# Kernel tuning notes

Hardware: AMD Instinct MI355X
Metric: run time of the kernel (lower is better)

Reference implementation:

```python
import jax, jax.numpy as jnp
from jax import lax
import numpy as np

B, S, HID = 1, 1024, 4096
H, D = 64, 64  # num_heads, head_size (hidden = H*D)


def setup_inputs() -> dict:
    key = jax.random.key(0)
    ks = jax.random.split(key, 14)
    s = 0.02  # weight init scale
    return {
        "hidden": jax.random.normal(ks[0], (B, S, HID), jnp.float32),
        "w_key": jax.random.normal(ks[1], (HID, HID), jnp.float32) * s,
        "w_value": jax.random.normal(ks[2], (HID, HID), jnp.float32) * s,
        "w_receptance": jax.random.normal(ks[3], (HID, HID), jnp.float32) * s,
        "w_gate": jax.random.normal(ks[4], (HID, HID), jnp.float32) * s,
        "w_output": jax.random.normal(ks[5], (HID, HID), jnp.float32) * s,
        "time_mix_key": jax.random.uniform(ks[6], (HID,), jnp.float32),
        "time_mix_value": jax.random.uniform(ks[7], (HID,), jnp.float32),
        "time_mix_receptance": jax.random.uniform(ks[8], (HID,), jnp.float32),
        "time_mix_gate": jax.random.uniform(ks[9], (HID,), jnp.float32),
        "time_decay": jax.random.normal(ks[10], (H, D), jnp.float32) * 0.5,
        "time_faaaa": jax.random.normal(ks[11], (H, D), jnp.float32) * 0.5,
        "gn_weight": jnp.ones((HID,), jnp.float32),
        "gn_bias": jnp.zeros((HID,), jnp.float32),
    }


def reference(hidden, w_key, w_value, w_receptance, w_gate, w_output,
              time_mix_key, time_mix_value, time_mix_receptance, time_mix_gate,
              time_decay, time_faaaa, gn_weight, gn_bias):
    b, s, hid = hidden.shape
    h, d = time_decay.shape

    # time_shift: shifted[t] = hidden[t-1], shifted[0] = 0 (state is None)
    shifted = jnp.concatenate([jnp.zeros_like(hidden[:, :1]), hidden[:, :-1]], axis=1)

    def mix(m):
        return hidden * m + shifted * (1.0 - m)

    k = mix(time_mix_key) @ w_key.T            # (b, s, hid)
    v = mix(time_mix_value) @ w_value.T
    r = mix(time_mix_receptance) @ w_receptance.T
    g = jax.nn.silu(mix(time_mix_gate) @ w_gate.T)

    def heads(x):  # (b, s, hid) -> (s, b, h, d) for scan over time
        return x.reshape(b, s, h, d).transpose(1, 0, 2, 3)

    kh, vh, rh = heads(k), heads(v), heads(r)

    td = jnp.exp(-jnp.exp(time_decay))[None, :, :, None]  # (1, h, d, 1)
    tf = time_faaaa[None, :, :, None]                      # (1, h, d, 1)

    def step(state, rkv):
        r_t, k_t, v_t = rkv                                # each (b, h, d)
        a = k_t[..., :, None] * v_t[..., None, :]          # (b, h, d, d) outer product
        o = jnp.einsum('bhd,bhde->bhe', r_t, tf * a + state)
        return a + td * state, o

    state0 = jnp.zeros((b, h, d, d), jnp.float32)
    _, out = lax.scan(step, state0, (rh, kh, vh))          # out: (s, b, h, d)
    out = out.transpose(1, 0, 2, 3).reshape(b, s, hid)

    # GroupNorm(num_groups=h, channels=hid) over flattened tokens
    x = out.reshape(b * s, h, d)
    mu = x.mean(-1, keepdims=True)
    var = x.var(-1, keepdims=True)
    xn = (x - mu) * lax.rsqrt(var + 1e-5)
    xn = xn.reshape(b * s, hid) * gn_weight + gn_bias
    xn = xn.reshape(b, s, hid)

    return (g * xn) @ w_output.T
```

## Files before the change

### kernel.cpp

```cpp
#include <hip/hip_runtime.h>

#define S_LEN 1024
#define HIDN  4096
#define NH    64
#define HD    64
#define NCH   32
#define CLEN  32
#define NKT   64

typedef short bf16x8 __attribute__((ext_vector_type(8)));
typedef float f32x4  __attribute__((ext_vector_type(4)));

__device__ __forceinline__ unsigned short f2bf(float x){
  unsigned u = __float_as_uint(x);
  u += 0x7fffu + ((u >> 16) & 1u);
  return (unsigned short)(u >> 16);
}

__device__ __forceinline__ void gload_lds16(const void* g, void* l){
  __builtin_amdgcn_global_load_lds(
      (const __attribute__((address_space(1))) void*)g,
      (__attribute__((address_space(3))) void*)l, 16, 0, 0);
}

#define SBAR() do { __builtin_amdgcn_sched_barrier(0); \
                    __builtin_amdgcn_s_barrier();      \
                    __builtin_amdgcn_sched_barrier(0); } while(0)
#define WAIT_LGKM0() do { asm volatile("s_waitcnt lgkmcnt(0)" ::: "memory"); \
                          __builtin_amdgcn_sched_barrier(0); } while(0)
#define WAIT_VM4()  do { asm volatile("s_waitcnt vmcnt(4)" ::: "memory"); \
                         __builtin_amdgcn_sched_barrier(0); } while(0)
#define WAIT_VM0()  do { asm volatile("s_waitcnt vmcnt(0)" ::: "memory"); \
                         __builtin_amdgcn_sched_barrier(0); } while(0)

__global__ __launch_bounds__(256)
void wconv_kernel(const float* __restrict__ w0, const float* __restrict__ w1,
                  const float* __restrict__ w2, const float* __restrict__ w3,
                  const float* __restrict__ w4, unsigned short* __restrict__ out)
{
  const int z = blockIdx.y;
  const float* __restrict__ w = (z==0)?w0:(z==1)?w1:(z==2)?w2:(z==3)?w3:w4;
  const size_t idx = (size_t)blockIdx.x * 2048 + (size_t)threadIdx.x * 8;
  float4 a = *(const float4*)(w + idx);
  float4 b = *(const float4*)(w + idx + 4);
  ushort4 lo, hi;
  lo.x = f2bf(a.x); lo.y = f2bf(a.y); lo.z = f2bf(a.z); lo.w = f2bf(a.w);
  hi.x = f2bf(b.x); hi.y = f2bf(b.y); hi.z = f2bf(b.z); hi.w = f2bf(b.w);
  unsigned short* o = out + (size_t)z * HIDN * HIDN + idx;
  *(ushort4*)(o)     = lo;
  *(ushort4*)(o + 4) = hi;
}

__global__ __launch_bounds__(256)
void mix_kernel(const float* __restrict__ hidden,
                const float* __restrict__ tmk, const float* __restrict__ tmv,
                const float* __restrict__ tmr, const float* __restrict__ tmg,
                unsigned short* __restrict__ mixed)
{
  int idx = blockIdx.x * 256 + threadIdx.x;
  int i = idx & (HIDN - 1);
  float h  = hidden[idx];
  float sh = (idx >= HIDN) ? hidden[idx - HIDN] : 0.f;
  float mk = tmk[i], mv = tmv[i], mr = tmr[i], mg = tmg[i];
  mixed[idx + 0 * S_LEN * HIDN] = f2bf(h * mk + sh * (1.f - mk));
  mixed[idx + 1 * S_LEN * HIDN] = f2bf(h * mv + sh * (1.f - mv));
  mixed[idx + 2 * S_LEN * HIDN] = f2bf(h * mr + sh * (1.f - mr));
  mixed[idx + 3 * S_LEN * HIDN] = f2bf(h * mg + sh * (1.f - mg));
}

__global__ __launch_bounds__(512, 2)
void gemm256(const unsigned short* __restrict__ Aall,
             const unsigned short* __restrict__ Wall,
             float* __restrict__ Call, int silu_mask)
{
  const int bid  = blockIdx.x;
  const int xcd  = bid & 7;
  const int slot = bid >> 3;
  const int nz   = xcd * 8 + (slot >> 2);
  const int mt   = slot & 3;
  const int z    = nz >> 4;
  const int nt   = nz & 15;
  const int m0 = mt * 256, n0 = nt * 256;

  const unsigned short* __restrict__ A = Aall + (size_t)z * S_LEN * HIDN;
  const unsigned short* __restrict__ W = Wall + (size_t)z * HIDN * HIDN;
  float* __restrict__ C = Call + (size_t)z * S_LEN * HIDN;

  __shared__ __align__(16) unsigned short As[2][2][128 * 64];
  __shared__ __align__(16) unsigned short Bs[2][2][128 * 64];

  const int tid  = threadIdx.x;
  const int lane = tid & 63;
  const int wid  = tid >> 6;
  const int wr   = wid >> 2;
  const int wc   = wid & 3;
  const int fr   = lane & 15;
  const int fku  = lane >> 4;
  const int cxA  = fku * 16;

  const int ob0 = tid * 16, ob1 = (512 + tid) * 16;
  const int r0 = ob0 >> 7, r1 = ob1 >> 7;
  const int cb0 = (ob0 & 127) ^ ((r0 & 7) << 4);
  const int cb1 = (ob1 & 127) ^ ((r1 & 7) << 4);
  const unsigned short* A0 = A + (size_t)(m0 + r0) * HIDN + (cb0 >> 1);
  const unsigned short* A1 = A + (size_t)(m0 + r1) * HIDN + (cb1 >> 1);
  const unsigned short* W0 = W + (size_t)(n0 + r0) * HIDN + (cb0 >> 1);
  const unsigned short* W1 = W + (size_t)(n0 + r1) * HIDN + (cb1 >> 1);
  const int lo0 = ob0 >> 1, lo1 = ob1 >> 1;

  f32x4 acc[8][4];
#pragma unroll
  for (int mi = 0; mi < 8; ++mi)
#pragma unroll
    for (int ni = 0; ni < 4; ++ni) acc[mi][ni] = (f32x4){0.f, 0.f, 0.f, 0.f};

  auto stageA = [&](int t, int h, int db) {
    gload_lds16(A0 + (size_t)h * 128 * HIDN + t * 64, &As[db][h][lo0]);
    gload_lds16(A1 + (size_t)h * 128 * HIDN + t * 64, &As[db][h][lo1]);
  };
  auto stageB = [&](int t, int h, int db) {
    gload_lds16(W0 + (size_t)h * 128 * HIDN + t * 64, &Bs[db][h][lo0]);
    gload_lds16(W1 + (size_t)h * 128 * HIDN + t * 64, &Bs[db][h][lo1]);
  };
  auto readA = [&](bf16x8 (&a)[2][4], int db, int mh) {
#pragma unroll
    for (int kk = 0; kk < 2; ++kk)
#pragma unroll
      for (int mi = 0; mi < 4; ++mi) {
        int rr  = mh * 64 + mi * 16 + fr;
        int byo = rr * 128 + ((kk * 64 + cxA) ^ ((rr & 7) << 4));
        a[kk][mi] = *(const bf16x8*)((const char*)As[db][wr] + byo);
      }
  };
  auto readB = [&](bf16x8 (&b)[2][2], int db, int nh) {
#pragma unroll
    for (int kk = 0; kk < 2; ++kk)
#pragma unroll
      for (int ni = 0; ni < 2; ++ni) {
        int rr  = (wc & 1) * 64 + nh * 32 + ni * 16 + fr;
        int byo = rr * 128 + ((kk * 64 + cxA) ^ ((rr & 7) << 4));
        b[kk][ni] = *(const bf16x8*)((const char*)Bs[db][wc >> 1] + byo);
      }
  };
  auto quad = [&](bf16x8 (&a)[2][4], bf16x8 (&b)[2][2], int mh, int nh) {
#pragma unroll
    for (int kk = 0; kk < 2; ++kk)
#pragma unroll
      for (int mi = 0; mi < 4; ++mi)
#pragma unroll
        for (int ni = 0; ni < 2; ++ni)
          acc[mh * 4 + mi][nh * 2 + ni] = __builtin_amdgcn_mfma_f32_16x16x32_bf16(
              a[kk][mi], b[kk][ni], acc[mh * 4 + mi][nh * 2 + ni], 0, 0, 0);
  };

  stageB(0, 0, 0); stageB(0, 1, 0);
  stageA(0, 0, 0); stageA(0, 1, 0);
  stageB(1, 0, 1); stageB(1, 1, 1);
  WAIT_VM4();
  SBAR();

  bf16x8 a8[2][4], b0[2][2], b1[2][2];

  for (int T = 0; T < NKT; ++T) {
    const int db  = T & 1;
    const int dbA = (T + 1) & 1;
    const int tA  = (T + 1 < NKT) ? T + 1 : NKT - 1;
    const int tB  = (T + 2 < NKT) ? T + 2 : NKT - 1;
    readA(a8, db, 0);
    readB(b0, db, 0);
    stageA(tA, 0, dbA);
    SBAR();
    WAIT_LGKM0();
    __builtin_amdgcn_s_setprio(1);
    quad(a8, b0, 0, 0);
    __builtin_amdgcn_s_setprio(0);
    SBAR();
    readB(b1, db, 1);
    stageA(tA, 1, dbA);
    SBAR();
    WAIT_LGKM0();
    __builtin_amdgcn_s_setprio(1);
    quad(a8, b1, 0, 1);
    __builtin_amdgcn_s_setprio(0);
    SBAR();
    readA(a8, db, 1);
    stageB(tB, 0, db);
    SBAR();
    WAIT_LGKM0();
    __builtin_amdgcn_s_setprio(1);
    quad(a8, b1, 1, 1);
    __builtin_amdgcn_s_setprio(0);
    SBAR();
    stageB(tB, 1, db);
    WAIT_VM4();
    SBAR();
    __builtin_amdgcn_s_setprio(1);
    quad(a8, b0, 1, 0);
    __builtin_amdgcn_s_setprio(0);
    SBAR();
  }
  WAIT_VM0();

  const bool do_silu = (silu_mask >> z) & 1;
  const int orow = fku * 4;
#pragma unroll
  for (int mi = 0; mi < 8; ++mi)
#pragma unroll
    for (int ni = 0; ni < 4; ++ni)
#pragma unroll
      for (int r = 0; r < 4; ++r) {
        int row = m0 + wr * 128 + mi * 16 + orow + r;
        int col = n0 + wc * 64 + ni * 16 + fr;
        float v = acc[mi][ni][r];
        if (do_silu) v = v / (1.f + __expf(-v));
        C[(size_t)row * HIDN + col] = v;
      }
}

__global__ __launch_bounds__(256)
void gemm_splitk(const unsigned short* __restrict__ A,
                 const unsigned short* __restrict__ W,
                 float* __restrict__ C)
{
  const int bid  = blockIdx.x;
  const int xcd  = bid & 7;
  const int slot = bid >> 3;
  const int mt   = slot & 7;
  const int nl   = (slot >> 3) & 3;
  const int ks   = slot >> 5;
  const int nt   = xcd * 4 + nl;
  const int m0 = mt * 128, n0 = nt * 128;
  const int kb = ks * (HIDN / 2), ke = kb + (HIDN / 2);

  __shared__ unsigned short As[2][128 * 32];
  __shared__ unsigned short Bs[2][128 * 32];

  const int tid  = threadIdx.x;
  const int lane = tid & 63;
  const int wave = tid >> 6;
  const int wr = (wave >> 1) * 64;
  const int wc = (wave & 1) * 64;
  const int fr = lane & 15;
  const int fk = (lane >> 4) * 8;

  const int q0 = tid, q1 = 256 + tid;
  const int r0 = q0 >> 2, c0 = (q0 & 3) * 8;
  const int r1 = q1 >> 2, c1 = (q1 & 3) * 8;
  const unsigned short* A0 = A + (size_t)(m0 + r0) * HIDN + c0;
  const unsigned short* A1 = A + (size_t)(m0 + r1) * HIDN + c1;
  const unsigned short* W0 = W + (size_t)(n0 + r0) * HIDN + c0;
  const unsigned short* W1 = W + (size_t)(n0 + r1) * HIDN + c1;

  f32x4 acc[4][4];
#pragma unroll
  for (int mi = 0; mi < 4; ++mi)
#pragma unroll
    for (int ni = 0; ni < 4; ++ni) acc[mi][ni] = (f32x4){0.f, 0.f, 0.f, 0.f};

  for (int k0 = kb; k0 < ke; k0 += 64) {
    gload_lds16(A0 + k0,      &As[0][q0 * 8]);
    gload_lds16(A1 + k0,      &As[0][q1 * 8]);
    gload_lds16(A0 + k0 + 32, &As[1][q0 * 8]);
    gload_lds16(A1 + k0 + 32, &As[1][q1 * 8]);
    gload_lds16(W0 + k0,      &Bs[0][q0 * 8]);
    gload_lds16(W1 + k0,      &Bs[0][q1 * 8]);
    gload_lds16(W0 + k0 + 32, &Bs[1][q0 * 8]);
    gload_lds16(W1 + k0 + 32, &Bs[1][q1 * 8]);
    __syncthreads();

#pragma unroll
    for (int kk = 0; kk < 2; ++kk) {
      bf16x8 af[4], bq[4];
#pragma unroll
      for (int mi = 0; mi < 4; ++mi)
        af[mi] = *(const bf16x8*)(&As[kk][(wr + mi * 16 + fr) * 32 + fk]);
#pragma unroll
      for (int ni = 0; ni < 4; ++ni)
        bq[ni] = *(const bf16x8*)(&Bs[kk][(wc + ni * 16 + fr) * 32 + fk]);
#pragma unroll
      for (int mi = 0; mi < 4; ++mi)
#pragma unroll
        for (int ni = 0; ni < 4; ++ni)
          acc[mi][ni] = __builtin_amdgcn_mfma_f32_16x16x32_bf16(af[mi], bq[ni], acc[mi][ni], 0, 0, 0);
    }
    __syncthreads();
  }

  const int orow = (lane >> 4) * 4;
#pragma unroll
  for (int mi = 0; mi < 4; ++mi)
#pragma unroll
    for (int ni = 0; ni < 4; ++ni)
#pragma unroll
      for (int r = 0; r < 4; ++r) {
        int row = m0 + wr + mi * 16 + orow + r;
        int col = n0 + wc + ni * 16 + fr;
        atomicAdd(&C[(size_t)row * HIDN + col], acc[mi][ni][r]);
      }
}

__global__ __launch_bounds__(64)
void rec_pass1(const float* __restrict__ kb, const float* __restrict__ vb,
               const float* __restrict__ time_decay, float* __restrict__ X)
{
  const int c = blockIdx.x, h = blockIdx.y, e = threadIdx.x;
  const float tde = __expf(-__expf(time_decay[h * 64 + e]));
  float td[64];
#pragma unroll
  for (int d = 0; d < 64; ++d) td[d] = __shfl(tde, d, 64);
  float st[64];
#pragma unroll
  for (int d = 0; d < 64; ++d) st[d] = 0.f;

  for (int t = c * CLEN; t < c * CLEN + CLEN; ++t) {
    const size_t off = (size_t)t * HIDN + h * 64;
    const float vl = vb[off + e];
    const float* __restrict__ krow = kb + off;
#pragma unroll
    for (int d = 0; d < 64; ++d)
      st[d] = fmaf(td[d], st[d], krow[d] * vl);
  }
#pragma unroll
  for (int d = 0; d < 64; ++d)
    X[(((size_t)c * NH + h) * 64 + d) * 64 + e] = st[d];
}

__global__ __launch_bounds__(64)
void rec_pass2(const float* __restrict__ time_decay,
               const float* __restrict__ X, float* __restrict__ Y)
{
  const int h = blockIdx.x, dq = blockIdx.y, e = threadIdx.x;
  float tdc[16];
#pragma unroll
  for (int i = 0; i < 16; ++i)
    tdc[i] = __expf(-(float)CLEN * __expf(time_decay[h * 64 + dq * 16 + i]));
  float acc[16];
#pragma unroll
  for (int i = 0; i < 16; ++i) acc[i] = 0.f;
  for (int c = 0; c < NCH; ++c) {
#pragma unroll
    for (int i = 0; i < 16; ++i) {
      size_t idx = (((size_t)c * NH + h) * 64 + dq * 16 + i) * 64 + e;
      Y[idx] = acc[i];
      acc[i] = fmaf(tdc[i], acc[i], X[idx]);
    }
  }
}

__global__ __launch_bounds__(64)
void rec_pass3(const float* __restrict__ kb, const float* __restrict__ vb,
               const float* __restrict__ rb, const float* __restrict__ gb,
               const float* __restrict__ time_decay, const float* __restrict__ time_faaaa,
               const float* __restrict__ gnw, const float* __restrict__ gnb,
               const float* __restrict__ Y, unsigned short* __restrict__ A2)
{
  const int c = blockIdx.x, h = blockIdx.y, e = threadIdx.x;
  const float tde = __expf(-__expf(time_decay[h * 64 + e]));
  float td[64];
#pragma unroll
  for (int d = 0; d < 64; ++d) td[d] = __shfl(tde, d, 64);
  float st[64];
#pragma unroll
  for (int d = 0; d < 64; ++d)
    st[d] = Y[(((size_t)c * NH + h) * 64 + d) * 64 + e];

  const float tf_l  = time_faaaa[h * 64 + e];
  const float gnw_l = gnw[h * 64 + e];
  const float gnb_l = gnb[h * 64 + e];

  for (int t = c * CLEN; t < c * CLEN + CLEN; ++t) {
    const size_t off = (size_t)t * HIDN + h * 64;
    const float kl = kb[off + e], rl = rb[off + e];
    const float vl = vb[off + e], gl = gb[off + e];

    float Asum = rl * tf_l * kl;
#pragma unroll
    for (int i = 1; i < 64; i <<= 1) Asum += __shfl_xor(Asum, i, 64);

    const float* __restrict__ krow = kb + off;
    const float* __restrict__ rrow = rb + off;
    float dot = 0.f;
#pragma unroll
    for (int d = 0; d < 64; ++d) {
      dot   = fmaf(rrow[d], st[d], dot);
      st[d] = fmaf(td[d], st[d], krow[d] * vl);
    }
    float o = fmaf(Asum, vl, dot);

    float s1 = o, s2 = o * o;
#pragma unroll
    for (int i = 1; i < 64; i <<= 1) {
      s1 += __shfl_xor(s1, i, 64);
      s2 += __shfl_xor(s2, i, 64);
    }
    float mean = s1 * (1.f / 64.f);
    float var  = s2 * (1.f / 64.f) - mean * mean;
    float xn   = (o - mean) * rsqrtf(var + 1e-5f);
    float yv   = xn * gnw_l + gnb_l;
    A2[off + e] = f2bf(gl * yv);
  }
}

extern "C" void kernel_launch(void* const* d_in, const int* in_sizes, int n_in,
                              void* d_out, int out_size, void* d_ws, size_t ws_size,
                              hipStream_t stream)
{
  const float* hidden     = (const float*)d_in[0];
  const float* w_key      = (const float*)d_in[1];
  const float* w_value    = (const float*)d_in[2];
  const float* w_recep    = (const float*)d_in[3];
  const float* w_gate     = (const float*)d_in[4];
  const float* w_output   = (const float*)d_in[5];
  const float* tmk        = (const float*)d_in[6];
  const float* tmv        = (const float*)d_in[7];
  const float* tmr        = (const float*)d_in[8];
  const float* tmg        = (const float*)d_in[9];
  const float* time_decay = (const float*)d_in[10];
  const float* time_faaaa = (const float*)d_in[11];
  const float* gnw        = (const float*)d_in[12];
  const float* gnb        = (const float*)d_in[13];
  float* out = (float*)d_out;

  char* ws = (char*)d_ws;
  unsigned short* wbf   = (unsigned short*)(ws);
  float*          Y     = (float*)(ws);
  unsigned short* mixed = (unsigned short*)(ws + 167772160);
  float*          X     = (float*)(ws + 167772160);
  float*          kvrg  = (float*)(ws + 201326592);
  unsigned short* A2    = (unsigned short*)(ws + 268435456);

  const float* kb = kvrg + 0 * (size_t)S_LEN * HIDN;
  const float* vb = kvrg + 1 * (size_t)S_LEN * HIDN;
  const float* rb = kvrg + 2 * (size_t)S_LEN * HIDN;
  const float* gb = kvrg + 3 * (size_t)S_LEN * HIDN;

  wconv_kernel<<<dim3(HIDN * HIDN / 2048, 5), 256, 0, stream>>>(
      w_key, w_value, w_recep, w_gate, w_output, wbf);

  mix_kernel<<<dim3(S_LEN * HIDN / 256), 256, 0, stream>>>(hidden, tmk, tmv, tmr, tmg, mixed);

  gemm256<<<dim3(256), 512, 0, stream>>>(mixed, wbf, kvrg, 0x8);

  rec_pass1<<<dim3(NCH, NH), 64, 0, stream>>>(kb, vb, time_decay, X);
  rec_pass2<<<dim3(NH, 4), 64, 0, stream>>>(time_decay, X, Y);
  rec_pass3<<<dim3(NCH, NH), 64, 0, stream>>>(kb, vb, rb, gb, time_decay, time_faaaa,
                                              gnw, gnb, Y, A2);

  hipMemsetAsync(d_out, 0, (size_t)out_size * sizeof(float), stream);
  gemm_splitk<<<dim3(512), 256, 0, stream>>>(A2, wbf + 4 * (size_t)HIDN * HIDN, out);
}
```

Measured before the change: 675.9 us.

## Reuse pipelined 256x256 GEMM body for split-K output projection and relax waits

Factors the 256x256 MFMA GEMM into a templated body that takes a K-tile count and an atomic-accumulate flag. The output projection now runs through it with 4-way split-K (16 K-tiles per block, atomicAdd epilogue), replacing the simpler 128x128 split-K kernel that synchronised twice per K step. The per-quad LDS waits and extra barriers in the main loop are removed and the vmcnt wait moves to the end of each iteration, aiming for more overlap of MFMA with LDS reads. Dropping the lgkmcnt waits leaves it to the compiler to place waits for the LDS reads, and the extra split-K partitions add atomic traffic.

New measurement: 690.3 us. 2.1% more time.

```diff
diff --git a/kernel.cpp b/kernel.cpp
--- a/kernel.cpp
+++ b/kernel.cpp
@@ -6,7 +6,6 @@
 #define HD    64
 #define NCH   32
 #define CLEN  32
-#define NKT   64
 
 typedef short bf16x8 __attribute__((ext_vector_type(8)));
 typedef float f32x4  __attribute__((ext_vector_type(4)));
@@ -26,12 +25,8 @@
 #define SBAR() do { __builtin_amdgcn_sched_barrier(0); \
                     __builtin_amdgcn_s_barrier();      \
                     __builtin_amdgcn_sched_barrier(0); } while(0)
-#define WAIT_LGKM0() do { asm volatile("s_waitcnt lgkmcnt(0)" ::: "memory"); \
-                          __builtin_amdgcn_sched_barrier(0); } while(0)
-#define WAIT_VM4()  do { asm volatile("s_waitcnt vmcnt(4)" ::: "memory"); \
-                         __builtin_amdgcn_sched_barrier(0); } while(0)
-#define WAIT_VM0()  do { asm volatile("s_waitcnt vmcnt(0)" ::: "memory"); \
-                         __builtin_amdgcn_sched_barrier(0); } while(0)
+#define WAIT_VM4()  do { asm volatile("s_waitcnt vmcnt(4)" ::: "memory"); } while(0)
+#define WAIT_VM0()  do { asm volatile("s_waitcnt vmcnt(0)" ::: "memory"); } while(0)
 
 __global__ __launch_bounds__(256)
 void wconv_kernel(const float* __restrict__ w0, const float* __restrict__ w1,
@@ -68,24 +63,11 @@
   mixed[idx + 3 * S_LEN * HIDN] = f2bf(h * mg + sh * (1.f - mg));
 }
 
-__global__ __launch_bounds__(512, 2)
-void gemm256(const unsigned short* __restrict__ Aall,
-             const unsigned short* __restrict__ Wall,
-             float* __restrict__ Call, int silu_mask)
-{
-  const int bid  = blockIdx.x;
-  const int xcd  = bid & 7;
-  const int slot = bid >> 3;
-  const int nz   = xcd * 8 + (slot >> 2);
-  const int mt   = slot & 3;
-  const int z    = nz >> 4;
-  const int nt   = nz & 15;
-  const int m0 = mt * 256, n0 = nt * 256;
-
-  const unsigned short* __restrict__ A = Aall + (size_t)z * S_LEN * HIDN;
-  const unsigned short* __restrict__ W = Wall + (size_t)z * HIDN * HIDN;
-  float* __restrict__ C = Call + (size_t)z * S_LEN * HIDN;
-
+template<int KTILES, bool ATOMIC>
+__device__ __forceinline__ void gemm_body(
+    const unsigned short* __restrict__ A, const unsigned short* __restrict__ W,
+    float* __restrict__ C, int m0, int n0, int kbase, bool do_silu)
+{
   __shared__ __align__(16) unsigned short As[2][2][128 * 64];
   __shared__ __align__(16) unsigned short Bs[2][2][128 * 64];
 
@@ -102,10 +84,10 @@
   const int r0 = ob0 >> 7, r1 = ob1 >> 7;
   const int cb0 = (ob0 & 127) ^ ((r0 & 7) << 4);
   const int cb1 = (ob1 & 127) ^ ((r1 & 7) << 4);
-  const unsigned short* A0 = A + (size_t)(m0 + r0) * HIDN + (cb0 >> 1);
-  const unsigned short* A1 = A + (size_t)(m0 + r1) * HIDN + (cb1 >> 1);
-  const unsigned short* W0 = W + (size_t)(n0 + r0) * HIDN + (cb0 >> 1);
-  const unsigned short* W1 = W + (size_t)(n0 + r1) * HIDN + (cb1 >> 1);
+  const unsigned short* A0 = A + (size_t)(m0 + r0) * HIDN + kbase + (cb0 >> 1);
+  const unsigned short* A1 = A + (size_t)(m0 + r1) * HIDN + kbase + (cb1 >> 1);
+  const unsigned short* W0 = W + (size_t)(n0 + r0) * HIDN + kbase + (cb0 >> 1);
+  const unsigned short* W1 = W + (size_t)(n0 + r1) * HIDN + kbase + (cb1 >> 1);
   const int lo0 = ob0 >> 1, lo1 = ob1 >> 1;
 
   f32x4 acc[8][4];
@@ -161,47 +143,39 @@
 
   bf16x8 a8[2][4], b0[2][2], b1[2][2];
 
-  for (int T = 0; T < NKT; ++T) {
+  for (int T = 0; T < KTILES; ++T) {
     const int db  = T & 1;
-    const int dbA = (T + 1) & 1;
-    const int tA  = (T + 1 < NKT) ? T + 1 : NKT - 1;
-    const int tB  = (T + 2 < NKT) ? T + 2 : NKT - 1;
+    const int dbA = db ^ 1;
+    const int tA  = (T + 1 < KTILES) ? T + 1 : T;
+    const int tB  = (T + 2 < KTILES) ? T + 2 : T;
     readA(a8, db, 0);
     readB(b0, db, 0);
     stageA(tA, 0, dbA);
-    SBAR();
-    WAIT_LGKM0();
     __builtin_amdgcn_s_setprio(1);
     quad(a8, b0, 0, 0);
     __builtin_amdgcn_s_setprio(0);
     SBAR();
     readB(b1, db, 1);
     stageA(tA, 1, dbA);
-    SBAR();
-    WAIT_LGKM0();
     __builtin_amdgcn_s_setprio(1);
     quad(a8, b1, 0, 1);
     __builtin_amdgcn_s_setprio(0);
     SBAR();
     readA(a8, db, 1);
     stageB(tB, 0, db);
-    SBAR();
-    WAIT_LGKM0();
     __builtin_amdgcn_s_setprio(1);
     quad(a8, b1, 1, 1);
     __builtin_amdgcn_s_setprio(0);
     SBAR();
     stageB(tB, 1, db);
-    WAIT_VM4();
-    SBAR();
     __builtin_amdgcn_s_setprio(1);
     quad(a8, b0, 1, 0);
     __builtin_amdgcn_s_setprio(0);
+    WAIT_VM4();
     SBAR();
   }
   WAIT_VM0();
 
-  const bool do_silu = (silu_mask >> z) & 1;
   const int orow = fku * 4;
 #pragma unroll
   for (int mi = 0; mi < 8; ++mi)
@@ -212,91 +186,45 @@
         int row = m0 + wr * 128 + mi * 16 + orow + r;
         int col = n0 + wc * 64 + ni * 16 + fr;
         float v = acc[mi][ni][r];
-        if (do_silu) v = v / (1.f + __expf(-v));
-        C[(size_t)row * HIDN + col] = v;
+        if (ATOMIC) {
+          atomicAdd(&C[(size_t)row * HIDN + col], v);
+        } else {
+          if (do_silu) v = v / (1.f + __expf(-v));
+          C[(size_t)row * HIDN + col] = v;
+        }
       }
 }
 
-__global__ __launch_bounds__(256)
-void gemm_splitk(const unsigned short* __restrict__ A,
-                 const unsigned short* __restrict__ W,
-                 float* __restrict__ C)
+__global__ __launch_bounds__(512, 2)
+void gemm_main(const unsigned short* __restrict__ Aall,
+               const unsigned short* __restrict__ Wall,
+               float* __restrict__ Call, int silu_mask)
 {
   const int bid  = blockIdx.x;
   const int xcd  = bid & 7;
   const int slot = bid >> 3;
-  const int mt   = slot & 7;
-  const int nl   = (slot >> 3) & 3;
-  const int ks   = slot >> 5;
-  const int nt   = xcd * 4 + nl;
-  const int m0 = mt * 128, n0 = nt * 128;
-  const int kb = ks * (HIDN / 2), ke = kb + (HIDN / 2);
-
-  __shared__ unsigned short As[2][128 * 32];
-  __shared__ unsigned short Bs[2][128 * 32];
-
-  const int tid  = threadIdx.x;
-  const int lane = tid & 63;
-  const int wave = tid >> 6;
-  const int wr = (wave >> 1) * 64;
-  const int wc = (wave & 1) * 64;
-  const int fr = lane & 15;
-  const int fk = (lane >> 4) * 8;
-
-  const int q0 = tid, q1 = 256 + tid;
-  const int r0 = q0 >> 2, c0 = (q0 & 3) * 8;
-  const int r1 = q1 >> 2, c1 = (q1 & 3) * 8;
-  const unsigned short* A0 = A + (size_t)(m0 + r0) * HIDN + c0;
-  const unsigned short* A1 = A + (size_t)(m0 + r1) * HIDN + c1;
-  const unsigned short* W0 = W + (size_t)(n0 + r0) * HIDN + c0;
-  const unsigned short* W1 = W + (size_t)(n0 + r1) * HIDN + c1;
-
-  f32x4 acc[4][4];
-#pragma unroll
-  for (int mi = 0; mi < 4; ++mi)
-#pragma unroll
-    for (int ni = 0; ni < 4; ++ni) acc[mi][ni] = (f32x4){0.f, 0.f, 0.f, 0.f};
-
-  for (int k0 = kb; k0 < ke; k0 += 64) {
-    gload_lds16(A0 + k0,      &As[0][q0 * 8]);
-    gload_lds16(A1 + k0,      &As[0][q1 * 8]);
-    gload_lds16(A0 + k0 + 32, &As[1][q0 * 8]);
-    gload_lds16(A1 + k0 + 32, &As[1][q1 * 8]);
-    gload_lds16(W0 + k0,      &Bs[0][q0 * 8]);
-    gload_lds16(W1 + k0,      &Bs[0][q1 * 8]);
-    gload_lds16(W0 + k0 + 32, &Bs[1][q0 * 8]);
-    gload_lds16(W1 + k0 + 32, &Bs[1][q1 * 8]);
-    __syncthreads();
-
-#pragma unroll
-    for (int kk = 0; kk < 2; ++kk) {
-      bf16x8 af[4], bq[4];
-#pragma unroll
-      for (int mi = 0; mi < 4; ++mi)
-        af[mi] = *(const bf16x8*)(&As[kk][(wr + mi * 16 + fr) * 32 + fk]);
-#pragma unroll
-      for (int ni = 0; ni < 4; ++ni)
-        bq[ni] = *(const bf16x8*)(&Bs[kk][(wc + ni * 16 + fr) * 32 + fk]);
-#pragma unroll
-      for (int mi = 0; mi < 4; ++mi)
-#pragma unroll
-        for (int ni = 0; ni < 4; ++ni)
-          acc[mi][ni] = __builtin_amdgcn_mfma_f32_16x16x32_bf16(af[mi], bq[ni], acc[mi][ni], 0, 0, 0);
-    }
-    __syncthreads();
-  }
-
-  const int orow = (lane >> 4) * 4;
-#pragma unroll
-  for (int mi = 0; mi < 4; ++mi)
-#pragma unroll
-    for (int ni = 0; ni < 4; ++ni)
-#pragma unroll
-      for (int r = 0; r < 4; ++r) {
-        int row = m0 + wr + mi * 16 + orow + r;
-        int col = n0 + wc + ni * 16 + fr;
-        atomicAdd(&C[(size_t)row * HIDN + col], acc[mi][ni][r]);
-      }
+  const int nz   = xcd * 8 + (slot >> 2);
+  const int mt   = slot & 3;
+  const int z    = nz >> 4;
+  const int nt   = nz & 15;
+  gemm_body<64, false>(Aall + (size_t)z * S_LEN * HIDN,
+                       Wall + (size_t)z * HIDN * HIDN,
+                       Call + (size_t)z * S_LEN * HIDN,
+                       mt * 256, nt * 256, 0, (silu_mask >> z) & 1);
+}
+
+__global__ __launch_bounds__(512, 2)
+void gemm_out(const unsigned short* __restrict__ A,
+              const unsigned short* __restrict__ W,
+              float* __restrict__ C)
+{
+  const int bid  = blockIdx.x;
+  const int xcd  = bid & 7;
+  const int slot = bid >> 3;
+  const int nt   = xcd * 2 + (slot & 1);
+  const int ks   = (slot >> 1) & 3;
+  const int mt   = (slot >> 3) & 3;
+  gemm_body<16, true>(A, W, C, mt * 256, nt * 256, ks * (HIDN / 4), false);
 }
 
 __global__ __launch_bounds__(64)
@@ -439,7 +367,7 @@
 
   mix_kernel<<<dim3(S_LEN * HIDN / 256), 256, 0, stream>>>(hidden, tmk, tmv, tmr, tmg, mixed);
 
-  gemm256<<<dim3(256), 512, 0, stream>>>(mixed, wbf, kvrg, 0x8);
+  gemm_main<<<dim3(256), 512, 0, stream>>>(mixed, wbf, kvrg, 0x8);
 
   rec_pass1<<<dim3(NCH, NH), 64, 0, stream>>>(kb, vb, time_decay, X);
   rec_pass2<<<dim3(NH, 4), 64, 0, stream>>>(time_decay, X, Y);
@@ -447,5 +375,5 @@
                                               gnw, gnb, Y, A2);
 
   hipMemsetAsync(d_out, 0, (size_t)out_size * sizeof(float), stream);
-  gemm_splitk<<<dim3(512), 256, 0, stream>>>(A2, wbf + 4 * (size_t)HIDN * HIDN, out);
-}
+  gemm_out<<<dim3(256), 512, 0, stream>>>(A2, wbf + 4 * (size_t)HIDN * HIDN, out);
+}
```
